# Kernel tuning notes

Hardware: AMD Instinct MI355X
Metric: run time of the kernel (lower is better)

Reference implementation:

```python
import jax, jax.numpy as jnp
from jax import lax
import numpy as np

GRID = 8
H384 = 6 * GRID * GRID  # 384, LSTM input and hidden size


def _conv(x, w, b):
    # x: [B,C,H,W], w: [O,I,kh,kw]
    y = lax.conv_general_dilated(x, w, (1, 1), 'VALID',
                                 dimension_numbers=('NCHW', 'OIHW', 'NCHW'))
    return y + b[None, :, None, None]


def _maxpool2(x):
    return lax.reduce_window(x, -jnp.inf, lax.max,
                             (1, 1, 2, 2), (1, 1, 2, 2), 'VALID')


def setup_inputs() -> dict:
    key = jax.random.key(0)
    ks = jax.random.split(key, 20)
    s = 0.05
    d = {
        'x': jax.random.normal(ks[0], (512, 100, 100), jnp.float32),
        # conv stack: Conv2d(1,16,7) ... Conv2d(128,128,3)
        'cw1': jax.random.normal(ks[1], (16, 1, 7, 7), jnp.float32) * s,
        'cb1': jnp.zeros((16,), jnp.float32),
        'cw2': jax.random.normal(ks[2], (32, 16, 4, 4), jnp.float32) * s,
        'cb2': jnp.zeros((32,), jnp.float32),
        'cw3': jax.random.normal(ks[3], (64, 32, 5, 5), jnp.float32) * s,
        'cb3': jnp.zeros((64,), jnp.float32),
        'cw4': jax.random.normal(ks[4], (128, 64, 5, 5), jnp.float32) * s,
        'cb4': jnp.zeros((128,), jnp.float32),
        'cw5': jax.random.normal(ks[5], (128, 128, 5, 5), jnp.float32) * s,
        'cb5': jnp.zeros((128,), jnp.float32),
        'cw6': jax.random.normal(ks[6], (128, 128, 3, 3), jnp.float32) * s,
        'cb6': jnp.zeros((128,), jnp.float32),
        # linear layers: 8192 -> 1024 -> 384, Sigmoid
        'lw1': jax.random.normal(ks[7], (1024, 8192), jnp.float32) * 0.01,
        'lb1': jnp.zeros((1024,), jnp.float32),
        'lw2': jax.random.normal(ks[8], (384, 1024), jnp.float32) * 0.02,
        'lb2': jnp.zeros((384,), jnp.float32),
        # LSTM (input 384, hidden 384, 1 layer), torch gate order i,f,g,o
        'w_ih': jax.random.normal(ks[9], (4 * H384, H384), jnp.float32) * s,
        'w_hh': jax.random.normal(ks[10], (4 * H384, H384), jnp.float32) * s,
        'b_ih': jnp.zeros((4 * H384,), jnp.float32),
        'b_hh': jnp.zeros((4 * H384,), jnp.float32),
    }
    return d


def reference(x, cw1, cb1, cw2, cb2, cw3, cb3, cw4, cb4, cw5, cb5, cw6, cb6,
              lw1, lb1, lw2, lb2, w_ih, w_hh, b_ih, b_hh):
    B = x.shape[0]
    h = x[:, None, :, :]                       # [B,1,100,100]
    h = _maxpool2(jax.nn.relu(_conv(h, cw1, cb1)))   # [B,16,47,47]
    h = _maxpool2(jax.nn.relu(_conv(h, cw2, cb2)))   # [B,32,22,22]
    h = jax.nn.relu(_conv(h, cw3, cb3))              # [B,64,18,18]
    h = jax.nn.relu(_conv(h, cw4, cb4))              # [B,128,14,14]
    h = jax.nn.relu(_conv(h, cw5, cb5))              # [B,128,10,10]
    h = jax.nn.relu(_conv(h, cw6, cb6))              # [B,128,8,8]
    h = h.reshape(B, -1)                             # [B,8192]
    h = h @ lw1.T + lb1                              # [B,1024]
    h = jax.nn.sigmoid(h @ lw2.T + lb2)              # [B,384]

    # Sequential LSTM over the batch dim with carried (h,c) state
    def step(carry, xt):
        hs, cs = carry
        gates = w_ih @ xt + b_ih + w_hh @ hs + b_hh  # [1536]
        i, f, g, o = jnp.split(gates, 4)
        cs = jax.nn.sigmoid(f) * cs + jax.nn.sigmoid(i) * jnp.tanh(g)
        hs = jax.nn.sigmoid(o) * jnp.tanh(cs)
        return (hs, cs), hs

    init = (jnp.zeros((H384,), x.dtype), jnp.zeros((H384,), x.dtype))
    _, ys = lax.scan(step, init, h)                  # [B,384]
    return ys.reshape(B, 6, GRID, GRID)
```

## Files before the change

### kernel.cpp

```cpp
#include <hip/hip_runtime.h>
#include <cstddef>
#include <cstdint>

#define T256 256

typedef __attribute__((ext_vector_type(8))) short bhalf8;
typedef __attribute__((ext_vector_type(4))) float floatx4;

__device__ __forceinline__ ushort f2bf(float f) {
  union { float f; uint32_t u; } v; v.f = f;
  return (ushort)((v.u + 0x7fffu + ((v.u >> 16) & 1u)) >> 16);
}

__global__ __launch_bounds__(256) void conv1_pool_k(
    const float* __restrict__ x, const float* __restrict__ w,
    const float* __restrict__ bias, float* __restrict__ out)
{
  __shared__ float img[10000];
  __shared__ float wsm[16 * 49];
  __shared__ float bsm[16];
  const int b = blockIdx.x, tid = threadIdx.x;
  for (int i = tid; i < 10000; i += T256) img[i] = x[(size_t)b * 10000 + i];
  for (int i = tid; i < 16 * 49; i += T256) wsm[i] = w[i];
  if (tid < 16) bsm[tid] = bias[tid];
  __syncthreads();
  for (int p = tid; p < 47 * 47; p += T256) {
    const int py = p / 47, px = p % 47;
    const int iy0 = 2 * py, ix0 = 2 * px;
    float win[8][8];
#pragma unroll
    for (int r = 0; r < 8; ++r)
#pragma unroll
      for (int c = 0; c < 8; ++c)
        win[r][c] = img[(iy0 + r) * 100 + (ix0 + c)];
#pragma unroll 1
    for (int oc = 0; oc < 16; ++oc) {
      float wr[49];
#pragma unroll
      for (int j = 0; j < 49; ++j) wr[j] = wsm[oc * 49 + j];
      float m = 0.f;
#pragma unroll
      for (int dy = 0; dy < 2; ++dy)
#pragma unroll
        for (int dx = 0; dx < 2; ++dx) {
          float s = bsm[oc];
#pragma unroll
          for (int ky = 0; ky < 7; ++ky)
#pragma unroll
            for (int kx = 0; kx < 7; ++kx)
              s += win[dy + ky][dx + kx] * wr[ky * 7 + kx];
          m = fmaxf(m, s);
        }
      out[((size_t)b * 16 + oc) * 2209 + p] = m;
    }
  }
}

__global__ __launch_bounds__(256) void wprep_k(
    const float* __restrict__ w, ushort* __restrict__ bswz,
    int IC, int KW, int OC, int total)
{
  const int idx = blockIdx.x * 256 + threadIdx.x;
  if (idx >= total) return;
  const int NT = OC / 16;
  const int lane = idx & 63;
  const int nt = (idx >> 6) % NT;
  const int ks = idx / (64 * NT);
  const int oc = nt * 16 + (lane & 15);
  const int kb = ks * 32 + (lane >> 4) * 8;
  ushort tmp[8];
#pragma unroll
  for (int j = 0; j < 8; ++j) {
    const int k = kb + j;
    const int ic = k % IC, tap = k / IC;
    tmp[j] = f2bf(w[((size_t)oc * IC + ic) * (KW * KW) + tap]);
  }
  *(bhalf8*)(bswz + (size_t)idx * 8) = *(const bhalf8*)tmp;
}

__global__ __launch_bounds__(256) void wprep_lin_k(
    const float* __restrict__ w, ushort* __restrict__ bswz,
    int Kdim, int NT, int total)
{
  const int idx = blockIdx.x * 256 + threadIdx.x;
  if (idx >= total) return;
  const int lane = idx & 63;
  const int nt = (idx >> 6) % NT;
  const int ks = idx / (64 * NT);
  const int oc = nt * 16 + (lane & 15);
  const int kb = ks * 32 + (lane >> 4) * 8;
  ushort tmp[8];
#pragma unroll
  for (int j = 0; j < 8; ++j) tmp[j] = f2bf(w[(size_t)oc * Kdim + kb + j]);
  *(bhalf8*)(bswz + (size_t)idx * 8) = *(const bhalf8*)tmp;
}

__global__ __launch_bounds__(256) void f2bf_k(
    const float* __restrict__ in, ushort* __restrict__ outv, int n)
{
  const int i = (blockIdx.x * 256 + threadIdx.x) * 4;
  if (i >= n) return;
  const float4 v = *(const float4*)&in[i];
  ushort tmp[4] = {f2bf(v.x), f2bf(v.y), f2bf(v.z), f2bf(v.w)};
  *(uint2*)&outv[i] = *(const uint2*)tmp;
}

__global__ __launch_bounds__(256) void conv2mfma_k(
    const float* __restrict__ in, const ushort* __restrict__ bswz,
    const float* __restrict__ bias, float* __restrict__ out)
{
  constexpr int IC = 16, IH = 47, IW = 47;
  constexpr int NPIX = IH * IW;
  constexpr int ROWU = IC + 8;
  constexpr int KS = 8;
  __shared__ ushort imgT[NPIX * ROWU];
  const int b = blockIdx.x, tid = threadIdx.x;
  const int lane = tid & 63, wv = tid >> 6;

  for (int e = tid; e < IC * NPIX; e += 256) {
    const int ic = e / NPIX, pix = e % NPIX;
    imgT[pix * ROWU + ic] = f2bf(in[((size_t)b * IC + ic) * NPIX + pix]);
  }
  __syncthreads();

  const int col = lane & 15, g = lane >> 4;
  const float b0 = bias[col], b1 = bias[16 + col];

  for (int it = wv; it < 66; it += 4) {
    const int pyp = it / 3, tx = it - pyp * 3;
    int px = tx * 16 + col; px = px < 43 ? px : 43;
    floatx4 acc[2][2];
#pragma unroll
    for (int dy = 0; dy < 2; ++dy)
#pragma unroll
      for (int nt = 0; nt < 2; ++nt) acc[dy][nt] = (floatx4){0.f, 0.f, 0.f, 0.f};

    for (int ks = 0; ks < KS; ++ks) {
      bhalf8 bf[2];
#pragma unroll
      for (int nt = 0; nt < 2; ++nt)
        bf[nt] = *(const bhalf8*)(bswz + ((size_t)(ks * 2 + nt) * 64 + lane) * 8);
      const int kk = ks * 32 + g * 8;
      const int tap = kk >> 4, icb = kk & 15;
      const int ky = tap >> 2, kx = tap & 3;
      bhalf8 af[2];
#pragma unroll
      for (int dy = 0; dy < 2; ++dy)
        af[dy] = *(const bhalf8*)&imgT[((2 * pyp + dy + ky) * IW + px + kx) * ROWU + icb];
#pragma unroll
      for (int dy = 0; dy < 2; ++dy)
#pragma unroll
        for (int nt = 0; nt < 2; ++nt)
          acc[dy][nt] = __builtin_amdgcn_mfma_f32_16x16x32_bf16(
              af[dy], bf[nt], acc[dy][nt], 0, 0, 0);
    }
#pragma unroll
    for (int nt = 0; nt < 2; ++nt) {
      const int oc = nt * 16 + col;
      const float bb = nt ? b1 : b0;
      float vv[4];
#pragma unroll
      for (int i = 0; i < 4; ++i) vv[i] = fmaxf(acc[0][nt][i], acc[1][nt][i]);
#pragma unroll
      for (int q = 0; q < 2; ++q) {
        const int pxp = tx * 8 + g * 2 + q;
        if (pxp < 22) {
          const float v = fmaxf(fmaxf(vv[2 * q], vv[2 * q + 1]) + bb, 0.f);
          out[((size_t)b * 32 + oc) * 484 + pyp * 22 + pxp] = v;
        }
      }
    }
  }
}

template <int IC, int IH, int IW, int KW_, int OC, int MC>
__global__ __launch_bounds__(256) void convmfma_k(
    const float* __restrict__ in, const ushort* __restrict__ bswz,
    const float* __restrict__ bias, float* __restrict__ out)
{
  constexpr int OH = IH - KW_ + 1, OW = IW - KW_ + 1, P = OH * OW;
  constexpr int NPIX = IH * IW;
  constexpr int KS = IC * KW_ * KW_ / 32;
  constexpr int NT = OC / 16;
  constexpr int NPW = NT / 4;
  constexpr int MT = (P + 15) / 16;
  constexpr int ROWU = IC + 8;
  static_assert(NT % 4 == 0 && IC % 32 == 0, "cfg");

  __shared__ ushort imgT[NPIX * ROWU];
  const int b = blockIdx.x, tid = threadIdx.x;
  const int lane = tid & 63, wv = tid >> 6;
  const int icoff = (lane >> 4) * 8;

  for (int e = tid; e < IC * NPIX; e += 256) {
    const int ic = e / NPIX, pix = e % NPIX;
    imgT[pix * ROWU + ic] = f2bf(in[((size_t)b * IC + ic) * NPIX + pix]);
  }
  __syncthreads();

  for (int m0 = 0; m0 < MT; m0 += MC) {
    floatx4 acc[MC][NPW];
#pragma unroll
    for (int mi = 0; mi < MC; ++mi)
#pragma unroll
      for (int nn = 0; nn < NPW; ++nn)
        acc[mi][nn] = (floatx4){0.f, 0.f, 0.f, 0.f};

    int pbase[MC];
#pragma unroll
    for (int mi = 0; mi < MC; ++mi) {
      int p = (m0 + mi) * 16 + (lane & 15);
      p = p < P ? p : P - 1;
      pbase[mi] = ((p / OW) * IW + (p % OW)) * ROWU;
    }

    bhalf8 bcur[NPW];
#pragma unroll
    for (int nn = 0; nn < NPW; ++nn)
      bcur[nn] = *(const bhalf8*)(bswz + ((size_t)(wv * NPW + nn) * 64 + lane) * 8);

    for (int ks = 0; ks < KS; ++ks) {
      bhalf8 bnext[NPW];
      if (ks + 1 < KS) {
#pragma unroll
        for (int nn = 0; nn < NPW; ++nn)
          bnext[nn] = *(const bhalf8*)(bswz +
              ((size_t)((ks + 1) * NT + wv * NPW + nn) * 64 + lane) * 8);
      }
      const int tap = (ks * 32) / IC;
      const int icb = (ks * 32) % IC;
      const int aoff = ((tap / KW_) * IW + (tap % KW_)) * ROWU + icb + icoff;
      bhalf8 af[MC];
#pragma unroll
      for (int mi = 0; mi < MC; ++mi)
        af[mi] = *(const bhalf8*)&imgT[pbase[mi] + aoff];
#pragma unroll
      for (int mi = 0; mi < MC; ++mi)
#pragma unroll
        for (int nn = 0; nn < NPW; ++nn)
          acc[mi][nn] = __builtin_amdgcn_mfma_f32_16x16x32_bf16(
              af[mi], bcur[nn], acc[mi][nn], 0, 0, 0);
      if (ks + 1 < KS) {
#pragma unroll
        for (int nn = 0; nn < NPW; ++nn) bcur[nn] = bnext[nn];
      }
    }
#pragma unroll
    for (int mi = 0; mi < MC; ++mi)
#pragma unroll
      for (int nn = 0; nn < NPW; ++nn) {
        const int oc = (wv * NPW + nn) * 16 + (lane & 15);
#pragma unroll
        for (int i = 0; i < 4; ++i) {
          const int p = (m0 + mi) * 16 + (lane >> 4) * 4 + i;
          if (p < P) {
            const float v = fmaxf(acc[mi][nn][i] + bias[oc], 0.f);
            out[((size_t)b * OC + oc) * P + p] = v;
          }
        }
      }
  }
}

__global__ __launch_bounds__(256) void gemm_bf16_k(
    const ushort* __restrict__ abf, const ushort* __restrict__ bswz,
    const float* __restrict__ bias, float* __restrict__ C,
    int M, int N, int K)
{
  __shared__ ushort As[64][72];
  const int bn = blockIdx.x, bm = blockIdx.y, tid = threadIdx.x;
  const int lane = tid & 63, wv = tid >> 6;
  const int m0 = bm * 64, n0 = bn * 64;
  const int NTg = N / 16;
  const int ntg = bn * 4 + wv;
  floatx4 acc[4];
#pragma unroll
  for (int mt = 0; mt < 4; ++mt) acc[mt] = (floatx4){0.f, 0.f, 0.f, 0.f};

  for (int kc = 0; kc < K / 64; ++kc) {
    __syncthreads();
#pragma unroll
    for (int q = 0; q < 2; ++q) {
      const int id = q * 256 + tid;
      const int row = id >> 3, kcol = (id & 7) * 8;
      *(bhalf8*)&As[row][kcol] =
          *(const bhalf8*)&abf[(size_t)(m0 + row) * K + kc * 64 + kcol];
    }
    __syncthreads();
#pragma unroll
    for (int k2 = 0; k2 < 2; ++k2) {
      const int ks = kc * 2 + k2;
      const bhalf8 bf = *(const bhalf8*)(bswz + ((size_t)(ks * NTg + ntg) * 64 + lane) * 8);
      const int ksub = k2 * 32 + (lane >> 4) * 8;
#pragma unroll
      for (int mt = 0; mt < 4; ++mt) {
        const bhalf8 af = *(const bhalf8*)&As[mt * 16 + (lane & 15)][ksub];
        acc[mt] = __builtin_amdgcn_mfma_f32_16x16x32_bf16(af, bf, acc[mt], 0, 0, 0);
      }
    }
  }
  const int n = n0 + wv * 16 + (lane & 15);
  const float bb = bias[n];
#pragma unroll
  for (int mt = 0; mt < 4; ++mt)
#pragma unroll
    for (int i = 0; i < 4; ++i) {
      const int m = m0 + mt * 16 + (lane >> 4) * 4 + i;
      C[(size_t)m * N + n] = acc[mt][i] + bb;
    }
}

template <int ACT>
__global__ __launch_bounds__(256) void gemm_tn_k(
    const float* __restrict__ A, const float* __restrict__ B,
    const float* __restrict__ b1, const float* __restrict__ b2,
    float* __restrict__ C, int M, int N, int K)
{
  __shared__ float As[32][66];
  __shared__ float Bs[32][36];
  const int bn = blockIdx.x, bm = blockIdx.y, tid = threadIdx.x;
  const int tx = tid & 7, ty = tid >> 3;
  const int m0 = bm * 64, n0 = bn * 32;
  double acc[2][4] = {{0, 0, 0, 0}, {0, 0, 0, 0}};
  for (int k0 = 0; k0 < K; k0 += 32) {
    __syncthreads();
#pragma unroll
    for (int l = 0; l < 8; ++l) {
      int id = tid + l * 256;
      int kk = id & 31, mm = id >> 5;
      As[kk][mm] = A[(size_t)(m0 + mm) * K + (k0 + kk)];
    }
#pragma unroll
    for (int l = 0; l < 4; ++l) {
      int id = tid + l * 256;
      int kk = id & 31, nn = id >> 5;
      Bs[kk][nn] = B[(size_t)(n0 + nn) * K + (k0 + kk)];
    }
    __syncthreads();
    float p[2][4] = {{0.f, 0.f, 0.f, 0.f}, {0.f, 0.f, 0.f, 0.f}};
#pragma unroll
    for (int kk = 0; kk < 32; ++kk) {
      const float2 av = *reinterpret_cast<const float2*>(&As[kk][ty * 2]);
      const float4 bv = *reinterpret_cast<const float4*>(&Bs[kk][tx * 4]);
      p[0][0] += av.x * bv.x; p[0][1] += av.x * bv.y;
      p[0][2] += av.x * bv.z; p[0][3] += av.x * bv.w;
      p[1][0] += av.y * bv.x; p[1][1] += av.y * bv.y;
      p[1][2] += av.y * bv.z; p[1][3] += av.y * bv.w;
    }
#pragma unroll
    for (int i = 0; i < 2; ++i)
#pragma unroll
      for (int j = 0; j < 4; ++j) acc[i][j] += (double)p[i][j];
  }
#pragma unroll
  for (int i = 0; i < 2; ++i) {
    const int m = m0 + ty * 2 + i;
#pragma unroll
    for (int j = 0; j < 4; ++j) {
      const int n = n0 + tx * 4 + j;
      double v = acc[i][j] + (double)b1[n];
      if (b2) v += (double)b2[n];
      if (ACT == 1) v = 1.0 / (1.0 + exp(-v));
      C[(size_t)m * N + n] = (float)v;
    }
  }
}

#define NWG 16
#define CPW 24
__global__ __launch_bounds__(768) void lstm_k(
    const float* __restrict__ gin, const float* __restrict__ whh,
    float* __restrict__ out, unsigned long long* __restrict__ tagged)
{
  __shared__ __align__(16) float hsm[8][52];
  __shared__ float gsum[96];
  const int wg = blockIdx.x, tid = threadIdx.x;
  const int r = tid >> 3, lk = tid & 7;
  const int gq = r / CPW, cl = r % CPW;
  const int grow = gq * 384 + wg * CPW + cl;
  float wreg[48];
  {
    const float* wr = whh + (size_t)grow * 384 + lk * 48;
#pragma unroll
    for (int i = 0; i < 48; ++i) wreg[i] = wr[i];
  }
  float c = 0.f;
  __syncthreads();
  for (int t = 0; t < 512; ++t) {
    float g0 = 0.f, g1 = 0.f, g2 = 0.f, g3 = 0.f;
    if (tid < CPW) {
      const int j = wg * CPW + tid;
      g0 = gin[(size_t)t * 1536 + 0 * 384 + j];
      g1 = gin[(size_t)t * 1536 + 1 * 384 + j];
      g2 = gin[(size_t)t * 1536 + 2 * 384 + j];
      g3 = gin[(size_t)t * 1536 + 3 * 384 + j];
    }
    if (tid < 384) {
      float hv;
      if (t == 0) {
        hv = 0.f;
      } else {
        unsigned long long u;
        do {
          u = __hip_atomic_load(&tagged[(size_t)(t - 1) * 384 + tid],
                                __ATOMIC_RELAXED, __HIP_MEMORY_SCOPE_AGENT);
        } while ((unsigned)(u >> 32) != (unsigned)t);
        union { unsigned ui; float f; } cv; cv.ui = (unsigned)u; hv = cv.f;
      }
      hsm[tid / 48][tid % 48] = hv;
    }
    __syncthreads();
    float s = 0.f;
    {
      const float4* hp = (const float4*)&hsm[lk][0];
#pragma unroll
      for (int q = 0; q < 12; ++q) {
        const float4 hv = hp[q];
        s += wreg[4 * q + 0] * hv.x + wreg[4 * q + 1] * hv.y
           + wreg[4 * q + 2] * hv.z + wreg[4 * q + 3] * hv.w;
      }
    }
    s += __shfl_xor(s, 1);
    s += __shfl_xor(s, 2);
    s += __shfl_xor(s, 4);
    if (lk == 0) gsum[r] = s;
    __syncthreads();
    if (tid < CPW) {
      const float gi = gsum[0 * CPW + tid] + g0;
      const float gf = gsum[1 * CPW + tid] + g1;
      const float gg = gsum[2 * CPW + tid] + g2;
      const float go = gsum[3 * CPW + tid] + g3;
      const float si = 1.f / (1.f + expf(-gi));
      const float sf = 1.f / (1.f + expf(-gf));
      const float so = 1.f / (1.f + expf(-go));
      c = sf * c + si * tanhf(gg);
      const float hn = so * tanhf(c);
      const int j = wg * CPW + tid;
      union { float f; unsigned ui; } cv; cv.f = hn;
      const unsigned long long pk = ((unsigned long long)(t + 1) << 32) | cv.ui;
      __hip_atomic_store(&tagged[(size_t)t * 384 + j], pk,
                         __ATOMIC_RELAXED, __HIP_MEMORY_SCOPE_AGENT);
      out[(size_t)t * 384 + j] = hn;
    }
  }
}

extern "C" void kernel_launch(void* const* d_in, const int* in_sizes, int n_in,
                              void* d_out, int out_size, void* d_ws, size_t ws_size,
                              hipStream_t stream)
{
  const float* x   = (const float*)d_in[0];
  const float* cw1 = (const float*)d_in[1];
  const float* cb1 = (const float*)d_in[2];
  const float* cw2 = (const float*)d_in[3];
  const float* cb2 = (const float*)d_in[4];
  const float* cw3 = (const float*)d_in[5];
  const float* cb3 = (const float*)d_in[6];
  const float* cw4 = (const float*)d_in[7];
  const float* cb4 = (const float*)d_in[8];
  const float* cw5 = (const float*)d_in[9];
  const float* cb5 = (const float*)d_in[10];
  const float* cw6 = (const float*)d_in[11];
  const float* cb6 = (const float*)d_in[12];
  const float* lw1 = (const float*)d_in[13];
  const float* lb1 = (const float*)d_in[14];
  const float* lw2 = (const float*)d_in[15];
  const float* lb2 = (const float*)d_in[16];
  const float* wih = (const float*)d_in[17];
  const float* whh = (const float*)d_in[18];
  const float* bih = (const float*)d_in[19];
  const float* bhh = (const float*)d_in[20];
  float* out = (float*)d_out;
  char* ws = (char*)d_ws;

  float* bufA = (float*)(ws);
  float* bufB = (float*)(ws + 72384512);
  float* l1o  = (float*)(ws + 123764736);
  float* x2   = (float*)(ws + 125861888);
  float* gin  = (float*)(ws + 126648320);
  ushort* bw3 = (ushort*)(ws + 123764736);
  ushort* bw4 = (ushort*)(ws + 123764736 + 102400);
  ushort* bw5 = (ushort*)(ws + 123764736 + 512000);
  ushort* bw6 = (ushort*)(ws + 123764736 + 1331200);
  ushort* bw2 = (ushort*)(ws + 123764736 + 1626112);
  ushort* bw1 = (ushort*)(ws);
  ushort* abf = (ushort*)(ws + 16777216);
  unsigned long long* tagged = (unsigned long long*)(ws + 25165824);

  wprep_k<<<(25 * 4 * 64 + 255) / 256, 256, 0, stream>>>(cw3, bw3, 32, 5, 64, 25 * 4 * 64);
  wprep_k<<<(50 * 8 * 64 + 255) / 256, 256, 0, stream>>>(cw4, bw4, 64, 5, 128, 50 * 8 * 64);
  wprep_k<<<(100 * 8 * 64 + 255) / 256, 256, 0, stream>>>(cw5, bw5, 128, 5, 128, 100 * 8 * 64);
  wprep_k<<<(36 * 8 * 64 + 255) / 256, 256, 0, stream>>>(cw6, bw6, 128, 3, 128, 36 * 8 * 64);
  wprep_k<<<(8 * 2 * 64 + 255) / 256, 256, 0, stream>>>(cw2, bw2, 16, 4, 32, 8 * 2 * 64);

  conv1_pool_k<<<512, 256, 0, stream>>>(x, cw1, cb1, bufA);
  conv2mfma_k<<<512, 256, 0, stream>>>(bufA, bw2, cb2, bufB);
  convmfma_k<32, 22, 22, 5, 64, 7><<<512, 256, 0, stream>>>(bufB, bw3, cb3, bufA);
  convmfma_k<64, 18, 18, 5, 128, 7><<<512, 256, 0, stream>>>(bufA, bw4, cb4, bufB);
  convmfma_k<128, 14, 14, 5, 128, 7><<<512, 256, 0, stream>>>(bufB, bw5, cb5, bufA);
  convmfma_k<128, 10, 10, 3, 128, 4><<<512, 256, 0, stream>>>(bufA, bw6, cb6, bufB);
  wprep_lin_k<<<(256 * 64 * 64 + 255) / 256, 256, 0, stream>>>(lw1, bw1, 8192, 64, 256 * 64 * 64);
  f2bf_k<<<(512 * 8192 / 4 + 255) / 256, 256, 0, stream>>>(bufB, abf, 512 * 8192);
  hipMemsetAsync(tagged, 0, 512 * 384 * 8, stream);
  gemm_bf16_k<<<dim3(16, 8), 256, 0, stream>>>(abf, bw1, lb1, l1o, 512, 1024, 8192);
  gemm_tn_k<1><<<dim3(384 / 32, 512 / 64), 256, 0, stream>>>(l1o, lw2, lb2, nullptr, x2, 512, 384, 1024);
  gemm_tn_k<0><<<dim3(1536 / 32, 512 / 64), 256, 0, stream>>>(x2, wih, bih, bhh, gin, 512, 1536, 384);
  lstm_k<<<NWG, 768, 0, stream>>>(gin, whh, out, tagged);
}
```

Before: 1.510 ms.

## Merge weight-prep launches, use fast LSTM activations, raise wave priority

Merges the five conv weight-swizzle kernels into one launch that dispatches on a flat index, removing four kernel launches. In the LSTM's sequential recurrence, the sigmoid and tanh calls switch to __expf-based approximations to shorten the per-step critical path. The first wave of each LSTM workgroup also gets raised scheduling priority so the gate-combining lanes run ahead. The fast math costs some accuracy, and the tanh formula may lose precision near zero.

```diff
diff --git a/kernel.cpp b/kernel.cpp
--- a/kernel.cpp
+++ b/kernel.cpp
@@ -10,6 +10,15 @@
 __device__ __forceinline__ ushort f2bf(float f) {
   union { float f; uint32_t u; } v; v.f = f;
   return (ushort)((v.u + 0x7fffu + ((v.u >> 16) & 1u)) >> 16);
+}
+
+__device__ __forceinline__ float fsig(float x) {
+  return 1.f / (1.f + __expf(-x));
+}
+__device__ __forceinline__ float ftanh(float x) {
+  const float e = __expf(-2.f * fabsf(x));
+  const float r = (1.f - e) / (1.f + e);
+  return copysignf(r, x);
 }
 
 __global__ __launch_bounds__(256) void conv1_pool_k(
@@ -56,12 +65,10 @@
   }
 }
 
-__global__ __launch_bounds__(256) void wprep_k(
+__device__ __forceinline__ void wprep_one(
     const float* __restrict__ w, ushort* __restrict__ bswz,
-    int IC, int KW, int OC, int total)
-{
-  const int idx = blockIdx.x * 256 + threadIdx.x;
-  if (idx >= total) return;
+    int IC, int KW, int OC, int idx)
+{
   const int NT = OC / 16;
   const int lane = idx & 63;
   const int nt = (idx >> 6) % NT;
@@ -76,6 +83,26 @@
     tmp[j] = f2bf(w[((size_t)oc * IC + ic) * (KW * KW) + tap]);
   }
   *(bhalf8*)(bswz + (size_t)idx * 8) = *(const bhalf8*)tmp;
+}
+
+__global__ __launch_bounds__(256) void wprep_all_k(
+    const float* __restrict__ cw2, const float* __restrict__ cw3,
+    const float* __restrict__ cw4, const float* __restrict__ cw5,
+    const float* __restrict__ cw6,
+    ushort* __restrict__ bw2, ushort* __restrict__ bw3,
+    ushort* __restrict__ bw4, ushort* __restrict__ bw5,
+    ushort* __restrict__ bw6)
+{
+  int idx = blockIdx.x * 256 + threadIdx.x;
+  if (idx < 6400)  { wprep_one(cw3, bw3, 32, 5, 64, idx); return; }
+  idx -= 6400;
+  if (idx < 25600) { wprep_one(cw4, bw4, 64, 5, 128, idx); return; }
+  idx -= 25600;
+  if (idx < 51200) { wprep_one(cw5, bw5, 128, 5, 128, idx); return; }
+  idx -= 51200;
+  if (idx < 18432) { wprep_one(cw6, bw6, 128, 3, 128, idx); return; }
+  idx -= 18432;
+  if (idx < 1024)  { wprep_one(cw2, bw2, 16, 4, 32, idx); }
 }
 
 __global__ __launch_bounds__(256) void wprep_lin_k(
@@ -385,6 +412,7 @@
     for (int i = 0; i < 48; ++i) wreg[i] = wr[i];
   }
   float c = 0.f;
+  if (tid < 64) __builtin_amdgcn_s_setprio(1);
   __syncthreads();
   for (int t = 0; t < 512; ++t) {
     float g0 = 0.f, g1 = 0.f, g2 = 0.f, g3 = 0.f;
@@ -430,11 +458,11 @@
       const float gf = gsum[1 * CPW + tid] + g1;
       const float gg = gsum[2 * CPW + tid] + g2;
       const float go = gsum[3 * CPW + tid] + g3;
-      const float si = 1.f / (1.f + expf(-gi));
-      const float sf = 1.f / (1.f + expf(-gf));
-      const float so = 1.f / (1.f + expf(-go));
-      c = sf * c + si * tanhf(gg);
-      const float hn = so * tanhf(c);
+      const float si = fsig(gi);
+      const float sf = fsig(gf);
+      const float so = fsig(go);
+      c = sf * c + si * ftanh(gg);
+      const float hn = so * ftanh(c);
       const int j = wg * CPW + tid;
       union { float f; unsigned ui; } cv; cv.f = hn;
       const unsigned long long pk = ((unsigned long long)(t + 1) << 32) | cv.ui;
@@ -487,11 +515,8 @@
   ushort* abf = (ushort*)(ws + 16777216);
   unsigned long long* tagged = (unsigned long long*)(ws + 25165824);
 
-  wprep_k<<<(25 * 4 * 64 + 255) / 256, 256, 0, stream>>>(cw3, bw3, 32, 5, 64, 25 * 4 * 64);
-  wprep_k<<<(50 * 8 * 64 + 255) / 256, 256, 0, stream>>>(cw4, bw4, 64, 5, 128, 50 * 8 * 64);
-  wprep_k<<<(100 * 8 * 64 + 255) / 256, 256, 0, stream>>>(cw5, bw5, 128, 5, 128, 100 * 8 * 64);
-  wprep_k<<<(36 * 8 * 64 + 255) / 256, 256, 0, stream>>>(cw6, bw6, 128, 3, 128, 36 * 8 * 64);
-  wprep_k<<<(8 * 2 * 64 + 255) / 256, 256, 0, stream>>>(cw2, bw2, 16, 4, 32, 8 * 2 * 64);
+  wprep_all_k<<<(102656 + 255) / 256, 256, 0, stream>>>(
+      cw2, cw3, cw4, cw5, cw6, bw2, bw3, bw4, bw5, bw6);
 
   conv1_pool_k<<<512, 256, 0, stream>>>(x, cw1, cb1, bufA);
   conv2mfma_k<<<512, 256, 0, stream>>>(bufA, bw2, cb2, bufB);
```

Result: faster. 1.428 ms (-5.5%).
